# Optimization experiments

Measured on AMD Instinct MI355X. Metric: run time of the kernel, lower is better.

The kernel has to match this reference:

```python
import jax, jax.numpy as jnp
import numpy as np

D_IN = 4096
D_OUT = 4096
EPS_NORM = 1e-6
EPS_Q = 1e-8


def _ternary_quantize(w):
    # per-output-channel absmean scale, then round/clamp to {-1,0,1}
    gamma = jnp.mean(jnp.abs(w), axis=-1)
    w_q = jnp.clip(jnp.round(w / (gamma[:, None] + EPS_Q)), -1.0, 1.0)
    return w_q, gamma


def setup_inputs() -> dict:
    key = jax.random.key(0)
    kx, kw = jax.random.split(key)
    x = jax.random.normal(kx, (2, 4096, D_IN), dtype=jnp.float32)
    # kaiming-uniform-like init then ternarize (mirrors torch __init__)
    bound = 1.0 / np.sqrt(D_IN)
    w_init = jax.random.uniform(kw, (D_OUT, D_IN), minval=-bound, maxval=bound, dtype=jnp.float32)
    w_q, gamma = _ternary_quantize(w_init)
    norm_weight = jnp.ones((D_IN,), dtype=jnp.float32)
    return {"x": x, "norm_weight": norm_weight, "w_q": w_q, "gamma": gamma}


def reference(x, norm_weight, w_q, gamma):
    # RMSNorm
    rms = jnp.sqrt(jnp.mean(x * x, axis=-1, keepdims=True) + EPS_NORM)
    xn = x / rms * norm_weight
    # ternary linear (dense fp32 GEMM, math identical to F.linear) + per-channel scale
    y = jnp.einsum('bsd,od->bso', xn, w_q) * gamma
    return y
```

## Files before the change

kernel.cpp:

```cpp
#include <hip/hip_runtime.h>
#include <hip/hip_bf16.h>
#include <stdint.h>

#define D_IN  4096
#define D_OUT 4096
#define MROWS 8192

using i32x4 = __attribute__((ext_vector_type(4))) int;

__global__ __launch_bounds__(256) void prep_kernel(
    const float* __restrict__ x, const float* __restrict__ nw,
    signed char* __restrict__ xq, float* __restrict__ srow,
    const float* __restrict__ wq, signed char* __restrict__ wb) {
  const int b = blockIdx.x;
  const int t = threadIdx.x;

  if (b < MROWS) {
    const float4* xr  = (const float4*)(x + (size_t)b * D_IN);
    const float4* nw4 = (const float4*)nw;

    float4 p[4];
    float ss = 0.f, mx = 0.f;
#pragma unroll
    for (int i = 0; i < 4; ++i) {
      const float4 v = xr[i * 256 + t];
      const float4 w = nw4[i * 256 + t];
      ss += v.x * v.x + v.y * v.y + v.z * v.z + v.w * v.w;
      p[i].x = v.x * w.x; p[i].y = v.y * w.y;
      p[i].z = v.z * w.z; p[i].w = v.w * w.w;
      mx = fmaxf(mx, fmaxf(fmaxf(fabsf(p[i].x), fabsf(p[i].y)),
                           fmaxf(fabsf(p[i].z), fabsf(p[i].w))));
    }
#pragma unroll
    for (int off = 32; off > 0; off >>= 1) {
      ss += __shfl_down(ss, off, 64);
      mx = fmaxf(mx, __shfl_down(mx, off, 64));
    }

    __shared__ float rs[4], rm[4];
    if ((t & 63) == 0) { rs[t >> 6] = ss; rm[t >> 6] = mx; }
    __syncthreads();
    const float scale =
        rsqrtf((rs[0] + rs[1] + rs[2] + rs[3]) * (1.0f / D_IN) + 1e-6f);
    const float rowmax = fmaxf(fmaxf(rm[0], rm[1]), fmaxf(rm[2], rm[3])) * scale;
    const float s   = fmaxf(rowmax, 1e-20f) * (1.0f / 127.0f);
    const float f   = scale / s;
    if (t == 0) srow[b] = s;

    int* out = (int*)(xq + (size_t)b * D_IN);
#pragma unroll
    for (int i = 0; i < 4; ++i) {
      const int q0 = (int)rintf(p[i].x * f);
      const int q1 = (int)rintf(p[i].y * f);
      const int q2 = (int)rintf(p[i].z * f);
      const int q3 = (int)rintf(p[i].w * f);
      out[i * 256 + t] =
          (q0 & 0xFF) | ((q1 & 0xFF) << 8) | ((q2 & 0xFF) << 16) | (q3 << 24);
    }
  } else {
    const int cb = b - MROWS;
    const float4* w4 = (const float4*)wq;
    int* o = (int*)wb;
#pragma unroll
    for (int i = 0; i < 4; ++i) {
      const int idx = cb * 1024 + i * 256 + t;
      const float4 v = w4[idx];
      const int q0 = (int)v.x, q1 = (int)v.y, q2 = (int)v.z, q3 = (int)v.w;
      o[idx] = (q0 & 0xFF) | ((q1 & 0xFF) << 8) | ((q2 & 0xFF) << 16) | (q3 << 24);
    }
  }
}

#define BM 256
#define BN 256
#define BKB 64
#define NKT (D_IN / BKB)
#define SLOT_BYTES (BM * BKB)

#define WVM(n_) asm volatile("s_waitcnt vmcnt(" #n_ ")" ::: "memory")
#define BAR()   __builtin_amdgcn_s_barrier()

#define STAGE(t_)                                                             \
  do {                                                                        \
    _Pragma("unroll") for (int _i = 0; _i < 2; ++_i)                          \
        __builtin_amdgcn_global_load_lds(                                     \
            (__attribute__((address_space(1))) void*)(A + aOff[_i] +          \
                                                      (t_) * BKB),            \
            (__attribute__((address_space(3))) void*)&sA[(t_) & 3]            \
                                                       [ldsOff[_i]],          \
            16, 0, 0);                                                        \
    _Pragma("unroll") for (int _i = 0; _i < 2; ++_i)                          \
        __builtin_amdgcn_global_load_lds(                                     \
            (__attribute__((address_space(1))) void*)(B + bOff[_i] +          \
                                                      (t_) * BKB),            \
            (__attribute__((address_space(3))) void*)&sB[(t_) & 3]            \
                                                       [ldsOff[_i]],          \
            16, 0, 0);                                                        \
  } while (0)

#define READF(t_, fa_, fb_)                                                   \
  do {                                                                        \
    _Pragma("unroll") for (int _i = 0; _i < 8; ++_i)                          \
        fa_[_i] = *(const i32x4*)&sA[(t_) & 3][aoff0 + _i * (16 * BKB)];      \
    _Pragma("unroll") for (int _j = 0; _j < 4; ++_j)                          \
        fb_[_j] = *(const i32x4*)&sB[(t_) & 3][boff0 + _j * (16 * BKB)];      \
  } while (0)

#define MFMA_C(fa_, fb_)                                                      \
  do {                                                                        \
    __builtin_amdgcn_s_setprio(1);                                            \
    _Pragma("unroll") for (int _i = 0; _i < 8; ++_i)                          \
        _Pragma("unroll") for (int _j = 0; _j < 4; ++_j)                      \
            acc[_i][_j] = __builtin_amdgcn_mfma_i32_16x16x64_i8(              \
                fa_[_i], fb_[_j], acc[_i][_j], 0, 0, 0);                      \
    __builtin_amdgcn_s_setprio(0);                                            \
  } while (0)

#define BODY(T_, fcA_, fcB_, fnA_, fnB_, STG_, WAIT_)                         \
  do {                                                                        \
    READF((T_) + 1, fnA_, fnB_);                                              \
    STG_;                                                                     \
    MFMA_C(fcA_, fcB_);                                                       \
    WAIT_;                                                                    \
    BAR();                                                                    \
  } while (0)

__global__ __launch_bounds__(512, 2) void gemm_kernel(
    const signed char* __restrict__ A,
    const signed char* __restrict__ B,
    const float* __restrict__ srow,
    const float* __restrict__ gamma,
    float* __restrict__ C) {
  __shared__ __align__(16) signed char sA[4][SLOT_BYTES];
  __shared__ __align__(16) signed char sB[4][SLOT_BYTES];

  const int tid  = threadIdx.x;
  const int lane = tid & 63;
  const int wv   = tid >> 6;
  const int wm   = wv >> 2;
  const int wn   = wv & 3;
  const int bn   = blockIdx.x;
  const int bm   = blockIdx.y;

  i32x4 acc[8][4];
#pragma unroll
  for (int i = 0; i < 8; ++i)
#pragma unroll
    for (int j = 0; j < 4; ++j) acc[i][j] = (i32x4){0, 0, 0, 0};

  size_t aOff[2], bOff[2];
  int ldsOff[2];
#pragma unroll
  for (int i = 0; i < 2; ++i) {
    const int c  = i * 512 + tid;
    const int r  = c >> 2;
    const int cc = ((c & 3) ^ ((r >> 1) & 3)) * 16;
    aOff[i] = (size_t)(bm * BM + r) * D_IN + cc;
    bOff[i] = (size_t)(bn * BN + r) * D_IN + cc;
    ldsOff[i] = (i * 512 + wv * 64) * 16;
  }

  const int kk    = (((lane >> 4) ^ ((lane >> 1) & 3))) * 16;
  const int aoff0 = (wm * 128 + (lane & 15)) * BKB + kk;
  const int boff0 = (wn * 64  + (lane & 15)) * BKB + kk;

  i32x4 f0a[8], f0b[4], f1a[8], f1b[4];

  STAGE(0); STAGE(1); STAGE(2);
  WVM(4);
  BAR();
  READF(0, f0a, f0b);

#pragma unroll 1
  for (int T = 0; T < NKT - 4; T += 2) {
    BODY(T,     f0a, f0b, f1a, f1b, STAGE(T + 3), WVM(4));
    BODY(T + 1, f1a, f1b, f0a, f0b, STAGE(T + 4), WVM(4));
  }
  BODY(60, f0a, f0b, f1a, f1b, STAGE(63), WVM(4));
  BODY(61, f1a, f1b, f0a, f0b, ,          WVM(0));
  READF(63, f1a, f1b);
  MFMA_C(f0a, f0b);
  MFMA_C(f1a, f1b);

  const int col0 = bn * BN + wn * 64 + (lane & 15);
  const int row0 = bm * BM + wm * 128 + ((lane >> 4) * 4);
  float g[4];
#pragma unroll
  for (int j = 0; j < 4; ++j) g[j] = gamma[col0 + j * 16];

#pragma unroll
  for (int i = 0; i < 8; ++i) {
#pragma unroll
    for (int r = 0; r < 4; ++r) {
      const int row = row0 + i * 16 + r;
      const float sr = srow[row];
#pragma unroll
      for (int j = 0; j < 4; ++j) {
        C[(size_t)row * D_OUT + col0 + j * 16] =
            (float)acc[i][j][r] * sr * g[j];
      }
    }
  }
}

#undef BODY
#undef MFMA_C
#undef READF
#undef STAGE
#undef WVM
#undef BAR

extern "C" void kernel_launch(void* const* d_in, const int* in_sizes, int n_in,
                              void* d_out, int out_size, void* d_ws, size_t ws_size,
                              hipStream_t stream) {
  const float* x     = (const float*)d_in[0];
  const float* nw    = (const float*)d_in[1];
  const float* wq    = (const float*)d_in[2];
  const float* gamma = (const float*)d_in[3];
  float* y = (float*)d_out;

  signed char* xq = (signed char*)d_ws;
  signed char* wb = xq + (size_t)MROWS * D_IN;
  float* srow = (float*)(wb + (size_t)D_OUT * D_IN);

  prep_kernel<<<MROWS + 4096, 256, 0, stream>>>(x, nw, xq, srow, wq, wb);

  gemm_kernel<<<dim3(D_OUT / BN, MROWS / BM), 512, 0, stream>>>(xq, wb, srow, gamma, y);
}
```

Measured before the change: 384.2 us.

## Switch int8 GEMM to 32x32x32 MFMA with static LDS slot indexing

Replaces the 16x16x64 int8 MFMA tiling with 32x32x32 MFMA instructions, so each wave computes a 128x64 tile with 8 larger accumulators and re-derives the swizzled LDS fragment offsets and epilogue row mapping. The main loop is unrolled by four so the LDS ring slot indices become compile-time constants, and a running k offset replaces the per-tile address arithmetic. The larger MFMA shape needs fewer instructions per tile and reads LDS fragments more efficiently, at the cost of a more complex fragment layout and epilogue whose correctness depends on the swizzle matching.

```diff
diff --git a/kernel.cpp b/kernel.cpp
--- a/kernel.cpp
+++ b/kernel.cpp
@@ -6,7 +6,8 @@
 #define D_OUT 4096
 #define MROWS 8192
 
-using i32x4 = __attribute__((ext_vector_type(4))) int;
+using i32x4  = __attribute__((ext_vector_type(4)))  int;
+using i32x16 = __attribute__((ext_vector_type(16))) int;
 
 __global__ __launch_bounds__(256) void prep_kernel(
     const float* __restrict__ x, const float* __restrict__ nw,
@@ -80,48 +81,50 @@
 #define WVM(n_) asm volatile("s_waitcnt vmcnt(" #n_ ")" ::: "memory")
 #define BAR()   __builtin_amdgcn_s_barrier()
 
-#define STAGE(t_)                                                             \
+#define STAGE(k0_, ss_)                                                       \
   do {                                                                        \
     _Pragma("unroll") for (int _i = 0; _i < 2; ++_i)                          \
         __builtin_amdgcn_global_load_lds(                                     \
-            (__attribute__((address_space(1))) void*)(A + aOff[_i] +          \
-                                                      (t_) * BKB),            \
-            (__attribute__((address_space(3))) void*)&sA[(t_) & 3]            \
-                                                       [ldsOff[_i]],          \
+            (__attribute__((address_space(1))) void*)(A + aOff[_i] + (k0_)),  \
+            (__attribute__((address_space(3))) void*)&sA[ss_][ldsOff[_i]],    \
             16, 0, 0);                                                        \
     _Pragma("unroll") for (int _i = 0; _i < 2; ++_i)                          \
         __builtin_amdgcn_global_load_lds(                                     \
-            (__attribute__((address_space(1))) void*)(B + bOff[_i] +          \
-                                                      (t_) * BKB),            \
-            (__attribute__((address_space(3))) void*)&sB[(t_) & 3]            \
-                                                       [ldsOff[_i]],          \
+            (__attribute__((address_space(1))) void*)(B + bOff[_i] + (k0_)),  \
+            (__attribute__((address_space(3))) void*)&sB[ss_][ldsOff[_i]],    \
             16, 0, 0);                                                        \
   } while (0)
 
-#define READF(t_, fa_, fb_)                                                   \
-  do {                                                                        \
-    _Pragma("unroll") for (int _i = 0; _i < 8; ++_i)                          \
-        fa_[_i] = *(const i32x4*)&sA[(t_) & 3][aoff0 + _i * (16 * BKB)];      \
-    _Pragma("unroll") for (int _j = 0; _j < 4; ++_j)                          \
-        fb_[_j] = *(const i32x4*)&sB[(t_) & 3][boff0 + _j * (16 * BKB)];      \
+#define READF(rs_, fa_, fb_)                                                  \
+  do {                                                                        \
+    _Pragma("unroll") for (int _i = 0; _i < 4; ++_i) {                        \
+      fa_[_i * 2]     = *(const i32x4*)&sA[rs_][aoff0 + _i * 2048 + ck0];     \
+      fa_[_i * 2 + 1] = *(const i32x4*)&sA[rs_][aoff0 + _i * 2048 + ck1];     \
+    }                                                                         \
+    _Pragma("unroll") for (int _j = 0; _j < 2; ++_j) {                        \
+      fb_[_j * 2]     = *(const i32x4*)&sB[rs_][boff0 + _j * 2048 + ck0];     \
+      fb_[_j * 2 + 1] = *(const i32x4*)&sB[rs_][boff0 + _j * 2048 + ck1];     \
+    }                                                                         \
   } while (0)
 
 #define MFMA_C(fa_, fb_)                                                      \
   do {                                                                        \
     __builtin_amdgcn_s_setprio(1);                                            \
-    _Pragma("unroll") for (int _i = 0; _i < 8; ++_i)                          \
-        _Pragma("unroll") for (int _j = 0; _j < 4; ++_j)                      \
-            acc[_i][_j] = __builtin_amdgcn_mfma_i32_16x16x64_i8(              \
-                fa_[_i], fb_[_j], acc[_i][_j], 0, 0, 0);                      \
+    _Pragma("unroll") for (int _ks = 0; _ks < 2; ++_ks)                       \
+        _Pragma("unroll") for (int _i = 0; _i < 4; ++_i)                      \
+            _Pragma("unroll") for (int _j = 0; _j < 2; ++_j)                  \
+                acc[_i][_j] = __builtin_amdgcn_mfma_i32_32x32x32_i8(          \
+                    fa_[_i * 2 + _ks], fb_[_j * 2 + _ks], acc[_i][_j],        \
+                    0, 0, 0);                                                 \
     __builtin_amdgcn_s_setprio(0);                                            \
   } while (0)
 
-#define BODY(T_, fcA_, fcB_, fnA_, fnB_, STG_, WAIT_)                         \
-  do {                                                                        \
-    READF((T_) + 1, fnA_, fnB_);                                              \
-    STG_;                                                                     \
+#define BODY(rs_, fcA_, fcB_, fnA_, fnB_, kofs_, ss_)                         \
+  do {                                                                        \
+    READF(rs_, fnA_, fnB_);                                                   \
+    STAGE(kb + (kofs_), ss_);                                                 \
     MFMA_C(fcA_, fcB_);                                                       \
-    WAIT_;                                                                    \
+    WVM(4);                                                                   \
     BAR();                                                                    \
   } while (0)
 
@@ -142,11 +145,11 @@
   const int bn   = blockIdx.x;
   const int bm   = blockIdx.y;
 
-  i32x4 acc[8][4];
-#pragma unroll
-  for (int i = 0; i < 8; ++i)
-#pragma unroll
-    for (int j = 0; j < 4; ++j) acc[i][j] = (i32x4){0, 0, 0, 0};
+  i32x16 acc[4][2];
+#pragma unroll
+  for (int i = 0; i < 4; ++i)
+#pragma unroll
+    for (int j = 0; j < 2; ++j) acc[i][j] = (i32x16){0};
 
   size_t aOff[2], bOff[2];
   int ldsOff[2];
@@ -160,45 +163,50 @@
     ldsOff[i] = (i * 512 + wv * 64) * 16;
   }
 
-  const int kk    = (((lane >> 4) ^ ((lane >> 1) & 3))) * 16;
-  const int aoff0 = (wm * 128 + (lane & 15)) * BKB + kk;
-  const int boff0 = (wn * 64  + (lane & 15)) * BKB + kk;
+  const int sxk   = (lane >> 1) & 3;
+  const int ck0   = (((lane >> 5)) ^ sxk) * 16;
+  const int ck1   = ((2 + (lane >> 5)) ^ sxk) * 16;
+  const int aoff0 = (wm * 128 + (lane & 31)) * BKB;
+  const int boff0 = (wn * 64  + (lane & 31)) * BKB;
 
   i32x4 f0a[8], f0b[4], f1a[8], f1b[4];
 
-  STAGE(0); STAGE(1); STAGE(2);
+  int kb = 0;
+  STAGE(0, 0); STAGE(BKB, 1); STAGE(2 * BKB, 2);
   WVM(4);
   BAR();
   READF(0, f0a, f0b);
 
 #pragma unroll 1
-  for (int T = 0; T < NKT - 4; T += 2) {
-    BODY(T,     f0a, f0b, f1a, f1b, STAGE(T + 3), WVM(4));
-    BODY(T + 1, f1a, f1b, f0a, f0b, STAGE(T + 4), WVM(4));
-  }
-  BODY(60, f0a, f0b, f1a, f1b, STAGE(63), WVM(4));
-  BODY(61, f1a, f1b, f0a, f0b, ,          WVM(0));
-  READF(63, f1a, f1b);
+  for (int T = 0; T < NKT - 4; T += 4) {
+    BODY(1, f0a, f0b, f1a, f1b, 3 * BKB, 3);
+    BODY(2, f1a, f1b, f0a, f0b, 4 * BKB, 0);
+    BODY(3, f0a, f0b, f1a, f1b, 5 * BKB, 1);
+    BODY(0, f1a, f1b, f0a, f0b, 6 * BKB, 2);
+    kb += 4 * BKB;
+  }
+  BODY(1, f0a, f0b, f1a, f1b, 3 * BKB, 3);
+  READF(2, f0a, f0b);
+  MFMA_C(f1a, f1b);
+  WVM(0);
+  BAR();
+  READF(3, f1a, f1b);
   MFMA_C(f0a, f0b);
   MFMA_C(f1a, f1b);
 
-  const int col0 = bn * BN + wn * 64 + (lane & 15);
-  const int row0 = bm * BM + wm * 128 + ((lane >> 4) * 4);
-  float g[4];
-#pragma unroll
-  for (int j = 0; j < 4; ++j) g[j] = gamma[col0 + j * 16];
-
-#pragma unroll
-  for (int i = 0; i < 8; ++i) {
-#pragma unroll
-    for (int r = 0; r < 4; ++r) {
-      const int row = row0 + i * 16 + r;
+  const int col0 = bn * BN + wn * 64 + (lane & 31);
+  const int rowb = bm * BM + wm * 128 + ((lane >> 5) * 4);
+  const float g0 = gamma[col0];
+  const float g1 = gamma[col0 + 32];
+
+#pragma unroll
+  for (int i = 0; i < 4; ++i) {
+#pragma unroll
+    for (int rr = 0; rr < 16; ++rr) {
+      const int row = rowb + i * 32 + (rr & 3) + 8 * (rr >> 2);
       const float sr = srow[row];
-#pragma unroll
-      for (int j = 0; j < 4; ++j) {
-        C[(size_t)row * D_OUT + col0 + j * 16] =
-            (float)acc[i][j][r] * sr * g[j];
-      }
+      C[(size_t)row * D_OUT + col0]      = (float)acc[i][0][rr] * sr * g0;
+      C[(size_t)row * D_OUT + col0 + 32] = (float)acc[i][1][rr] * sr * g1;
     }
   }
 }
```

Result: slower. 407.0 us (+5.9%).

## Use wave-per-row RMSNorm prep and stagger MFMA/LDS phases across wave groups

Applied to the files above, without the earlier changes.

The prep kernel now gives each 64-lane wave its own row, so the reduction needs only xor-shuffles and no shared-memory barrier, and it launches four times fewer blocks. In the GEMM main loop, waves with wm=1 issue their MFMAs before the LDS fragment reads and global staging, while wm=0 waves keep the original order. This skew is meant to interleave matrix-core and LDS/VMEM activity across the two wave groups. It costs higher register use in prep (16 float4 per lane) and duplicates the loop code in the GEMM.

```diff
diff --git a/kernel.cpp b/kernel.cpp
--- a/kernel.cpp
+++ b/kernel.cpp
@@ -15,50 +15,57 @@
   const int b = blockIdx.x;
   const int t = threadIdx.x;
 
-  if (b < MROWS) {
-    const float4* xr  = (const float4*)(x + (size_t)b * D_IN);
+  if (b < 2048) {
+    const int lane = t & 63;
+    const int row  = b * 4 + (t >> 6);
+    const float4* xr  = (const float4*)(x + (size_t)row * D_IN);
     const float4* nw4 = (const float4*)nw;
 
-    float4 p[4];
+    float4 p[16];
     float ss = 0.f, mx = 0.f;
 #pragma unroll
-    for (int i = 0; i < 4; ++i) {
-      const float4 v = xr[i * 256 + t];
-      const float4 w = nw4[i * 256 + t];
-      ss += v.x * v.x + v.y * v.y + v.z * v.z + v.w * v.w;
-      p[i].x = v.x * w.x; p[i].y = v.y * w.y;
-      p[i].z = v.z * w.z; p[i].w = v.w * w.w;
-      mx = fmaxf(mx, fmaxf(fmaxf(fabsf(p[i].x), fabsf(p[i].y)),
-                           fmaxf(fabsf(p[i].z), fabsf(p[i].w))));
-    }
-#pragma unroll
-    for (int off = 32; off > 0; off >>= 1) {
-      ss += __shfl_down(ss, off, 64);
-      mx = fmaxf(mx, __shfl_down(mx, off, 64));
-    }
-
-    __shared__ float rs[4], rm[4];
-    if ((t & 63) == 0) { rs[t >> 6] = ss; rm[t >> 6] = mx; }
-    __syncthreads();
-    const float scale =
-        rsqrtf((rs[0] + rs[1] + rs[2] + rs[3]) * (1.0f / D_IN) + 1e-6f);
-    const float rowmax = fmaxf(fmaxf(rm[0], rm[1]), fmaxf(rm[2], rm[3])) * scale;
-    const float s   = fmaxf(rowmax, 1e-20f) * (1.0f / 127.0f);
-    const float f   = scale / s;
-    if (t == 0) srow[b] = s;
-
-    int* out = (int*)(xq + (size_t)b * D_IN);
-#pragma unroll
-    for (int i = 0; i < 4; ++i) {
+    for (int c = 0; c < 4; ++c) {
+      float4 v[4], w[4];
+#pragma unroll
+      for (int i = 0; i < 4; ++i) {
+        v[i] = xr[(c * 4 + i) * 64 + lane];
+        w[i] = nw4[(c * 4 + i) * 64 + lane];
+      }
+#pragma unroll
+      for (int i = 0; i < 4; ++i) {
+        ss += v[i].x * v[i].x + v[i].y * v[i].y +
+              v[i].z * v[i].z + v[i].w * v[i].w;
+        float4 pp;
+        pp.x = v[i].x * w[i].x; pp.y = v[i].y * w[i].y;
+        pp.z = v[i].z * w[i].z; pp.w = v[i].w * w[i].w;
+        p[c * 4 + i] = pp;
+        mx = fmaxf(mx, fmaxf(fmaxf(fabsf(pp.x), fabsf(pp.y)),
+                             fmaxf(fabsf(pp.z), fabsf(pp.w))));
+      }
+    }
+#pragma unroll
+    for (int off = 1; off < 64; off <<= 1) {
+      ss += __shfl_xor(ss, off, 64);
+      mx = fmaxf(mx, __shfl_xor(mx, off, 64));
+    }
+    const float scale  = rsqrtf(ss * (1.0f / D_IN) + 1e-6f);
+    const float rowmax = mx * scale;
+    const float s = fmaxf(rowmax, 1e-20f) * (1.0f / 127.0f);
+    const float f = scale / s;
+    if (lane == 0) srow[row] = s;
+
+    int* out = (int*)(xq + (size_t)row * D_IN);
+#pragma unroll
+    for (int i = 0; i < 16; ++i) {
       const int q0 = (int)rintf(p[i].x * f);
       const int q1 = (int)rintf(p[i].y * f);
       const int q2 = (int)rintf(p[i].z * f);
       const int q3 = (int)rintf(p[i].w * f);
-      out[i * 256 + t] =
+      out[i * 64 + lane] =
           (q0 & 0xFF) | ((q1 & 0xFF) << 8) | ((q2 & 0xFF) << 16) | (q3 << 24);
     }
   } else {
-    const int cb = b - MROWS;
+    const int cb = b - 2048;
     const float4* w4 = (const float4*)wq;
     int* o = (int*)wb;
 #pragma unroll
@@ -116,11 +123,20 @@
     __builtin_amdgcn_s_setprio(0);                                            \
   } while (0)
 
-#define BODY(T_, fcA_, fcB_, fnA_, fnB_, STG_, WAIT_)                         \
+#define BODY_A(T_, fcA_, fcB_, fnA_, fnB_, STG_, WAIT_)                       \
   do {                                                                        \
     READF((T_) + 1, fnA_, fnB_);                                              \
     STG_;                                                                     \
     MFMA_C(fcA_, fcB_);                                                       \
+    WAIT_;                                                                    \
+    BAR();                                                                    \
+  } while (0)
+
+#define BODY_B(T_, fcA_, fcB_, fnA_, fnB_, STG_, WAIT_)                       \
+  do {                                                                        \
+    MFMA_C(fcA_, fcB_);                                                       \
+    READF((T_) + 1, fnA_, fnB_);                                              \
+    STG_;                                                                     \
     WAIT_;                                                                    \
     BAR();                                                                    \
   } while (0)
@@ -171,13 +187,23 @@
   BAR();
   READF(0, f0a, f0b);
 
+  if (wm) {
 #pragma unroll 1
-  for (int T = 0; T < NKT - 4; T += 2) {
-    BODY(T,     f0a, f0b, f1a, f1b, STAGE(T + 3), WVM(4));
-    BODY(T + 1, f1a, f1b, f0a, f0b, STAGE(T + 4), WVM(4));
-  }
-  BODY(60, f0a, f0b, f1a, f1b, STAGE(63), WVM(4));
-  BODY(61, f1a, f1b, f0a, f0b, ,          WVM(0));
+    for (int T = 0; T < NKT - 4; T += 2) {
+      BODY_B(T,     f0a, f0b, f1a, f1b, STAGE(T + 3), WVM(4));
+      BODY_B(T + 1, f1a, f1b, f0a, f0b, STAGE(T + 4), WVM(4));
+    }
+    BODY_B(60, f0a, f0b, f1a, f1b, STAGE(63), WVM(4));
+    BODY_B(61, f1a, f1b, f0a, f0b, ,          WVM(0));
+  } else {
+#pragma unroll 1
+    for (int T = 0; T < NKT - 4; T += 2) {
+      BODY_A(T,     f0a, f0b, f1a, f1b, STAGE(T + 3), WVM(4));
+      BODY_A(T + 1, f1a, f1b, f0a, f0b, STAGE(T + 4), WVM(4));
+    }
+    BODY_A(60, f0a, f0b, f1a, f1b, STAGE(63), WVM(4));
+    BODY_A(61, f1a, f1b, f0a, f0b, ,          WVM(0));
+  }
   READF(63, f1a, f1b);
   MFMA_C(f0a, f0b);
   MFMA_C(f1a, f1b);
@@ -203,7 +229,8 @@
   }
 }
 
-#undef BODY
+#undef BODY_A
+#undef BODY_B
 #undef MFMA_C
 #undef READF
 #undef STAGE
@@ -223,7 +250,7 @@
   signed char* wb = xq + (size_t)MROWS * D_IN;
   float* srow = (float*)(wb + (size_t)D_OUT * D_IN);
 
-  prep_kernel<<<MROWS + 4096, 256, 0, stream>>>(x, nw, xq, srow, wq, wb);
+  prep_kernel<<<2048 + 4096, 256, 0, stream>>>(x, nw, xq, srow, wq, wb);
 
   gemm_kernel<<<dim3(D_OUT / BN, MROWS / BM), 512, 0, stream>>>(xq, wb, srow, gamma, y);
 }
```

Result: no change. 383.0 us (-0.3%).
